# Kernel optimization log

Hardware: AMD Instinct MI355X
Metric: run time of the kernel (lower is better)

The kernel has to match this reference:

```python
import jax, jax.numpy as jnp
import numpy as np

NUM_MIXTURES = 10
DIM_INPUT = 512
DIM_FEATURES = 512
SEQ_LEN = 512
BATCH = 16
NUM_CHAR = 1024
DIM_CONTEXT = 256


def setup_inputs() -> dict:
    key = jax.random.key(0)
    ks = jax.random.split(key, 6)
    inputs = jax.random.normal(ks[0], (SEQ_LEN, BATCH, DIM_INPUT), dtype=jnp.float32)
    context_vectors = jax.random.normal(ks[1], (NUM_CHAR, BATCH, DIM_CONTEXT), dtype=jnp.float32)
    init_means = jnp.zeros((BATCH, NUM_MIXTURES), dtype=jnp.float32)
    # StackedLinearLayers params: 2 layers, leaky_relu between, out dim = 3*K
    s1 = 1.0 / np.sqrt(DIM_INPUT)
    s2 = 1.0 / np.sqrt(DIM_FEATURES)
    W1 = jax.random.uniform(ks[2], (DIM_INPUT, DIM_FEATURES), jnp.float32, -s1, s1)
    b1 = jax.random.uniform(ks[3], (DIM_FEATURES,), jnp.float32, -s1, s1)
    W2 = jax.random.uniform(ks[4], (DIM_FEATURES, 3 * NUM_MIXTURES), jnp.float32, -s2, s2)
    b2 = jax.random.uniform(ks[5], (3 * NUM_MIXTURES,), jnp.float32, -s2, s2)
    return dict(inputs=inputs, context_vectors=context_vectors, init_means=init_means,
                W1=W1, b1=b1, W2=W2, b2=b2, extra_chars=0)


def reference(inputs, context_vectors, init_means, W1, b1, W2, b2, extra_chars):
    K = NUM_MIXTURES
    seq_len, batch, _ = inputs.shape
    num_char = context_vectors.shape[0]
    total_char = num_char + extra_chars

    # StackedLinearLayers: leaky_relu MLP, last layer linear -> (S, B, 3K)
    h = jax.nn.leaky_relu(inputs @ W1 + b1, negative_slope=0.01)
    outs = h @ W2 + b2
    outs = jax.nn.softplus(outs)  # pos_fun = softplus

    delta_means, vars_, weights = jnp.split(outs, 3, axis=2)  # each (S, B, K)
    delta_means = delta_means / 25.0
    vars_ = jnp.clip(vars_, 0.01, 100.0)
    means = jnp.cumsum(delta_means, axis=0) + init_means[None, :, :]  # (S, B, K)

    cidxs = jnp.arange(total_char, dtype=jnp.float32)  # (T,)
    # dists: (S, B, K, T)
    dists = -((means[..., None] - cidxs) ** 2) * vars_[..., None]
    # attn_weights = exp(logsumexp over mixtures)
    attn_weights = jnp.exp(
        jax.scipy.special.logsumexp(jnp.log(weights)[..., None] + dists, axis=2)
    )  # (S, B, T)

    # attended contexts: (S, B, D)
    attn_contexts = jnp.einsum('sbc,cbd->sbd', attn_weights[:, :, :num_char], context_vectors)
    return attn_contexts, attn_weights, means, vars_, weights
```

## Files before the change

kernel.cpp:

```cpp
#include <hip/hip_runtime.h>
#include <math.h>

#define S_LEN 512
#define BATCH 16
#define DIN   512
#define DF    512
#define NMIX  10
#define NCHAR 1024
#define DCTX  256
#define M_ROWS (S_LEN*BATCH)

#define OFF_CTXOUT 0
#define OFF_ATTN   (S_LEN*BATCH*DCTX)
#define OFF_MEANS  (OFF_ATTN + S_LEN*BATCH*NCHAR)
#define OFF_VARS   (OFF_MEANS + S_LEN*BATCH*NMIX)
#define OFF_WTS    (OFF_VARS  + S_LEN*BATCH*NMIX)

#define WS_XH    0
#define WS_W1H   (8u<<20)
#define WS_W2T   (9u<<20)
#define WS_HH    (10u<<20)
#define WS_CTXH  (18u<<20)
#define WS_ATTNH (26u<<20)

#define NX4     1048576
#define NW14    65536
#define NCTX4   1048576
#define CVT4    (NX4 + NW14 + NCTX4)
#define CVT_BLOCKS (CVT4/256)
#define W2T_BLOCKS 64

typedef float    f32x16 __attribute__((ext_vector_type(16)));
typedef _Float16 f16x8  __attribute__((ext_vector_type(8)));

__device__ __forceinline__ unsigned short f2h(float x) {
    union { _Float16 h; unsigned short u; } cv;
    cv.h = (_Float16)x;
    return cv.u;
}
__device__ __forceinline__ ushort4 cvt4(float4 v) {
    ushort4 o; o.x = f2h(v.x); o.y = f2h(v.y); o.z = f2h(v.z); o.w = f2h(v.w);
    return o;
}

__global__ __launch_bounds__(256) void convert_kernel(
    const float* __restrict__ X, const float* __restrict__ W1,
    const float* __restrict__ ctx, const float* __restrict__ W2,
    unsigned short* __restrict__ Xh, unsigned short* __restrict__ W1h,
    unsigned short* __restrict__ ctxh, float* __restrict__ W2T)
{
    const int bid = blockIdx.x;
    if (bid < CVT_BLOCKS) {
        const int i4 = bid*256 + threadIdx.x;
        if (i4 < NX4) {
            ((ushort4*)Xh)[i4] = cvt4(((const float4*)X)[i4]);
        } else if (i4 < NX4 + NW14) {
            ((ushort4*)W1h)[i4 - NX4] = cvt4(((const float4*)W1)[i4 - NX4]);
        } else {
            const int j = i4 - NX4 - NW14;
            ((ushort4*)ctxh)[j] = cvt4(((const float4*)ctx)[j]);
        }
    } else {
        const int idx = (bid - CVT_BLOCKS)*256 + threadIdx.x;
        if (idx < 512*32) {
            const int j = idx >> 9, k = idx & 511;
            W2T[idx] = (j < 30) ? W2[k*30 + j] : 0.f;
        }
    }
}

__global__ __launch_bounds__(256) void gemm1_kernel(
    const unsigned short* __restrict__ Xh, const unsigned short* __restrict__ W1h,
    const float* __restrict__ b1, unsigned short* __restrict__ Hh)
{
    __shared__ __align__(16) unsigned short As[64*72];
    __shared__ __align__(16) unsigned short Bs[64*72];
    const int row0 = (blockIdx.x >> 3) * 64;
    const int n0   = (blockIdx.x & 7)  * 64;
    const int tid  = threadIdx.x;
    const int lane = tid & 63, w = tid >> 6;
    const int wr = (w >> 1) * 32, wc = (w & 1) * 32;
    const int m  = lane & 31,  g  = lane >> 5;
    const int sa = tid >> 2,   ka = (tid & 3) * 16;
    const int kb = tid & 63,   wb = tid >> 6;

    f32x16 acc = {};

    for (int kt = 0; kt < DIN; kt += 64) {
        uint4 av0 = *(const uint4*)(Xh  + (size_t)(row0+sa)*DIN + kt + ka);
        uint4 av1 = *(const uint4*)(Xh  + (size_t)(row0+sa)*DIN + kt + ka + 8);
        uint4 bv0 = *(const uint4*)(W1h + (size_t)(kt+kb)*DF + n0 + wb*16);
        uint4 bv1 = *(const uint4*)(W1h + (size_t)(kt+kb)*DF + n0 + wb*16 + 8);
        __syncthreads();
        *(uint4*)(As + sa*72 + ka)     = av0;
        *(uint4*)(As + sa*72 + ka + 8) = av1;
        {
            union { uint4 u; unsigned short s[8]; } p0, p1;
            p0.u = bv0; p1.u = bv1;
            #pragma unroll
            for (int i = 0; i < 8; i++) Bs[(wb*16 + i)*72 + kb]     = p0.s[i];
            #pragma unroll
            for (int i = 0; i < 8; i++) Bs[(wb*16 + 8 + i)*72 + kb] = p1.s[i];
        }
        __syncthreads();
        #pragma unroll
        for (int ks = 0; ks < 64; ks += 16) {
            f16x8 af = *(const f16x8*)(As + (wr+m)*72 + ks + g*8);
            f16x8 bf = *(const f16x8*)(Bs + (wc+m)*72 + ks + g*8);
            acc = __builtin_amdgcn_mfma_f32_32x32x16_f16(af, bf, acc, 0, 0, 0);
        }
    }
    const int ncol = n0 + wc + m;
    const float bb = b1[ncol];
    #pragma unroll
    for (int r = 0; r < 16; r++) {
        const int rowloc = (r & 3) + 8*(r >> 2) + 4*g;
        const int row = row0 + wr + rowloc;
        float v = acc[r] + bb;
        v = v > 0.f ? v : 0.01f * v;
        Hh[(size_t)row*DF + ncol] = f2h(v);
    }
}

__global__ __launch_bounds__(256) void gemm2_kernel(
    const unsigned short* __restrict__ Hh, const float* __restrict__ W2T,
    const float* __restrict__ b2,
    float* __restrict__ dmeans, float* __restrict__ dvars, float* __restrict__ dwts)
{
    __shared__ __align__(16) unsigned short Hs[32*520];
    const int tid = threadIdx.x;
    const int r0  = blockIdx.x * 32;
    {
        const uint4* src = (const uint4*)(Hh + (size_t)r0*DF);
        #pragma unroll
        for (int i = 0; i < 8; i++) {
            int u   = tid + i*256;
            int row = u >> 6;
            int col = (u & 63) * 8;
            *(uint4*)(Hs + row*520 + col) = src[u];
        }
    }
    __syncthreads();

    const int r  = tid & 31;
    const int j0 = tid >> 5;
    const unsigned short* hrow = Hs + r*520;
    float acc[4] = {0.f, 0.f, 0.f, 0.f};

    for (int k0 = 0; k0 < DF; k0 += 8) {
        union { uint4 u; _Float16 h[8]; } hv;
        hv.u = *(const uint4*)(hrow + k0);
        float wv[4][8];
        #pragma unroll
        for (int q = 0; q < 4; q++) {
            *(float4*)(wv[q])     = *(const float4*)(W2T + (size_t)(j0 + q*8)*DF + k0);
            *(float4*)(wv[q] + 4) = *(const float4*)(W2T + (size_t)(j0 + q*8)*DF + k0 + 4);
        }
        #pragma unroll
        for (int i = 0; i < 8; i++) {
            float hf = (float)hv.h[i];
            acc[0] = fmaf(hf, wv[0][i], acc[0]);
            acc[1] = fmaf(hf, wv[1][i], acc[1]);
            acc[2] = fmaf(hf, wv[2][i], acc[2]);
            acc[3] = fmaf(hf, wv[3][i], acc[3]);
        }
    }
    const int row = r0 + r;
    #pragma unroll
    for (int q = 0; q < 4; q++) {
        const int j = j0 + q*8;
        if (j >= 30) continue;
        float dot = acc[q] + b2[j];
        float sp  = fmaxf(dot, 0.f) + log1pf(__expf(-fabsf(dot)));
        if (j < 10)       dmeans[row*NMIX + j]      = sp / 25.0f;
        else if (j < 20)  dvars [row*NMIX + (j-10)] = fminf(fmaxf(sp, 0.01f), 100.f);
        else              dwts  [row*NMIX + (j-20)] = sp;
    }
}

__global__ __launch_bounds__(512) void scan_kernel(
    const float* __restrict__ init_means, float* __restrict__ means)
{
    const int p    = blockIdx.x;
    const int s    = threadIdx.x;
    const int lane = s & 63;
    const int wid  = s >> 6;

    float x = means[s*(BATCH*NMIX) + p];
    #pragma unroll
    for (int d = 1; d < 64; d <<= 1) {
        float tv = __shfl_up(x, d, 64);
        if (lane >= d) x += tv;
    }
    __shared__ float wsum[8];
    if (lane == 63) wsum[wid] = x;
    __syncthreads();
    float off = init_means[p];
    for (int i = 0; i < wid; i++) off += wsum[i];
    x += off;
    means[s*(BATCH*NMIX) + p] = x;
}

__global__ __launch_bounds__(256) void attn_kernel(
    const float* __restrict__ means, const float* __restrict__ vars,
    const float* __restrict__ wts,   float* __restrict__ attn,
    unsigned short* __restrict__ attnh)
{
    const int row = blockIdx.x;
    const int tid = threadIdx.x;
    float m[NMIX], v[NMIX], w[NMIX];
    #pragma unroll
    for (int k = 0; k < NMIX; k++) {
        m[k] = means[row*NMIX + k];
        v[k] = vars [row*NMIX + k];
        w[k] = wts  [row*NMIX + k];
    }
    const int t0 = tid * 4;
    float o[4];
    #pragma unroll
    for (int i = 0; i < 4; i++) {
        const float t = (float)(t0 + i);
        float sum = 0.f;
        #pragma unroll
        for (int k = 0; k < NMIX; k++) {
            float d = t - m[k];
            sum += w[k] * __expf(-d*d*v[k]);
        }
        o[i] = sum;
    }
    *(float4*)(attn + (size_t)row*NCHAR + t0) = make_float4(o[0],o[1],o[2],o[3]);
    ushort4 h; h.x = f2h(o[0]); h.y = f2h(o[1]); h.z = f2h(o[2]); h.w = f2h(o[3]);
    *(ushort4*)(attnh + (size_t)row*NCHAR + t0) = h;
}

__global__ __launch_bounds__(256) void ctx_mfma_kernel(
    const unsigned short* __restrict__ attnh, const unsigned short* __restrict__ ctxh,
    float* __restrict__ out)
{
    __shared__ __align__(16) unsigned short As[64*72];
    __shared__ __align__(16) unsigned short Bs[64*72];
    const int bid  = blockIdx.x;
    const int b    = bid >> 5;
    const int rem  = bid & 31;
    const int s0   = (rem >> 2) * 64;
    const int d0   = (rem & 3)  * 64;
    const int tid  = threadIdx.x;
    const int lane = tid & 63, w = tid >> 6;
    const int wr = (w >> 1) * 32, wc = (w & 1) * 32;
    const int m  = lane & 31,  g  = lane >> 5;
    const int sl = tid >> 2,   tq = (tid & 3) * 16;
    const int tb = tid & 63,   db = (tid >> 6) * 16;

    f32x16 acc = {};
    const unsigned short* abase = attnh + (size_t)(s0+sl)*(BATCH*NCHAR) + b*NCHAR + tq;
    const unsigned short* bbase = ctxh  + (size_t)b*DCTX + d0 + db;

    for (int kt = 0; kt < NCHAR; kt += 64) {
        uint4 a0 = *(const uint4*)(abase + kt);
        uint4 a1 = *(const uint4*)(abase + kt + 8);
        uint4 bv0 = *(const uint4*)(bbase + (size_t)(kt+tb)*(BATCH*DCTX));
        uint4 bv1 = *(const uint4*)(bbase + (size_t)(kt+tb)*(BATCH*DCTX) + 8);
        __syncthreads();
        *(uint4*)(As + sl*72 + tq)     = a0;
        *(uint4*)(As + sl*72 + tq + 8) = a1;
        {
            union { uint4 u; unsigned short s[8]; } p0, p1;
            p0.u = bv0; p1.u = bv1;
            #pragma unroll
            for (int i = 0; i < 8; i++) Bs[(db + i)*72 + tb]     = p0.s[i];
            #pragma unroll
            for (int i = 0; i < 8; i++) Bs[(db + 8 + i)*72 + tb] = p1.s[i];
        }
        __syncthreads();
        #pragma unroll
        for (int ks = 0; ks < 64; ks += 16) {
            f16x8 af = *(const f16x8*)(As + (wr+m)*72 + ks + g*8);
            f16x8 bf = *(const f16x8*)(Bs + (wc+m)*72 + ks + g*8);
            acc = __builtin_amdgcn_mfma_f32_32x32x16_f16(af, bf, acc, 0, 0, 0);
        }
    }
    #pragma unroll
    for (int r = 0; r < 16; r++) {
        int rowloc = (r & 3) + 8*(r >> 2) + 4*g;
        int s = s0 + wr + rowloc;
        out[(size_t)s*(BATCH*DCTX) + b*DCTX + d0 + wc + m] = acc[r];
    }
}

extern "C" void kernel_launch(void* const* d_in, const int* in_sizes, int n_in,
                              void* d_out, int out_size, void* d_ws, size_t ws_size,
                              hipStream_t stream)
{
    const float* X     = (const float*)d_in[0];
    const float* ctx   = (const float*)d_in[1];
    const float* initm = (const float*)d_in[2];
    const float* W1    = (const float*)d_in[3];
    const float* b1    = (const float*)d_in[4];
    const float* W2    = (const float*)d_in[5];
    const float* b2    = (const float*)d_in[6];

    float* out      = (float*)d_out;
    float* out_ctx  = out + OFF_CTXOUT;
    float* out_attn = out + OFF_ATTN;
    float* out_mean = out + OFF_MEANS;
    float* out_var  = out + OFF_VARS;
    float* out_wts  = out + OFF_WTS;

    char* ws = (char*)d_ws;
    unsigned short* Xh    = (unsigned short*)(ws + WS_XH);
    unsigned short* W1h   = (unsigned short*)(ws + WS_W1H);
    float*          W2T   = (float*)         (ws + WS_W2T);
    unsigned short* Hh    = (unsigned short*)(ws + WS_HH);
    unsigned short* ctxh  = (unsigned short*)(ws + WS_CTXH);
    unsigned short* attnh = (unsigned short*)(ws + WS_ATTNH);

    convert_kernel<<<CVT_BLOCKS + W2T_BLOCKS, 256, 0, stream>>>(
        X, W1, ctx, W2, Xh, W1h, ctxh, W2T);
    gemm1_kernel<<<(M_ROWS/64)*(DF/64), 256, 0, stream>>>(Xh, W1h, b1, Hh);
    gemm2_kernel<<<M_ROWS/32, 256, 0, stream>>>(Hh, W2T, b2, out_mean, out_var, out_wts);
    scan_kernel<<<BATCH*NMIX, 512, 0, stream>>>(initm, out_mean);
    attn_kernel<<<M_ROWS, 256, 0, stream>>>(out_mean, out_var, out_wts, out_attn, attnh);
    ctx_mfma_kernel<<<16*8*4, 256, 0, stream>>>(attnh, ctxh, out_ctx);
}
```

Measured before the change: 172.1 us.

## Fuse cumulative-sum scan into attention kernel, recomputing the scan per block

Removes the separate scan kernel and the old per-row attention kernel, replacing them with one kernel per (batch, 32-char tile). Each block loads the deltas, vars and weights for all 512 sequence steps of its batch, performs the prefix scan itself, stages the parameters in shared memory and computes attention for its char tile. This drops one launch and the global round trip for the means. In exchange the scan is recomputed redundantly 32 times per batch, and the attn stores become 4-byte and 2-byte scalars with only 32-element contiguity.

```diff
diff --git a/kernel.cpp b/kernel.cpp
--- a/kernel.cpp
+++ b/kernel.cpp
@@ -22,6 +22,7 @@
 #define WS_HH    (10u<<20)
 #define WS_CTXH  (18u<<20)
 #define WS_ATTNH (26u<<20)
+#define WS_DELTA (44u<<20)
 
 #define NX4     1048576
 #define NW14    65536
@@ -125,7 +126,7 @@
 __global__ __launch_bounds__(256) void gemm2_kernel(
     const unsigned short* __restrict__ Hh, const float* __restrict__ W2T,
     const float* __restrict__ b2,
-    float* __restrict__ dmeans, float* __restrict__ dvars, float* __restrict__ dwts)
+    float* __restrict__ deltas, float* __restrict__ dvars, float* __restrict__ dwts)
 {
     __shared__ __align__(16) unsigned short Hs[32*520];
     const int tid = threadIdx.x;
@@ -172,65 +173,100 @@
         if (j >= 30) continue;
         float dot = acc[q] + b2[j];
         float sp  = fmaxf(dot, 0.f) + log1pf(__expf(-fabsf(dot)));
-        if (j < 10)       dmeans[row*NMIX + j]      = sp / 25.0f;
+        if (j < 10)       deltas[row*NMIX + j]      = sp / 25.0f;
         else if (j < 20)  dvars [row*NMIX + (j-10)] = fminf(fmaxf(sp, 0.01f), 100.f);
         else              dwts  [row*NMIX + (j-20)] = sp;
     }
 }
 
-__global__ __launch_bounds__(512) void scan_kernel(
-    const float* __restrict__ init_means, float* __restrict__ means)
-{
-    const int p    = blockIdx.x;
-    const int s    = threadIdx.x;
-    const int lane = s & 63;
-    const int wid  = s >> 6;
-
-    float x = means[s*(BATCH*NMIX) + p];
-    #pragma unroll
-    for (int d = 1; d < 64; d <<= 1) {
-        float tv = __shfl_up(x, d, 64);
-        if (lane >= d) x += tv;
-    }
-    __shared__ float wsum[8];
-    if (lane == 63) wsum[wid] = x;
+__global__ __launch_bounds__(512) void attn_fused_kernel(
+    const float* __restrict__ deltas, const float* __restrict__ initm,
+    const float* __restrict__ vars_g, const float* __restrict__ wts_g,
+    float* __restrict__ means_out, float* __restrict__ attn,
+    unsigned short* __restrict__ attnh)
+{
+    __shared__ __align__(16) float mvw[256*36];
+    __shared__ float wsum[8][NMIX];
+    const int bid  = blockIdx.x;
+    const int b    = bid >> 5;
+    const int tc   = bid & 31;
+    const int tid  = threadIdx.x;
+    const int lane = tid & 63, wid = tid >> 6;
+    const int row  = tid*BATCH + b;
+
+    float d[NMIX], vv[NMIX], ww[NMIX];
+    #pragma unroll
+    for (int k = 0; k < NMIX; k++) d[k]  = deltas[row*NMIX + k];
+    #pragma unroll
+    for (int k = 0; k < NMIX; k++) vv[k] = vars_g[row*NMIX + k];
+    #pragma unroll
+    for (int k = 0; k < NMIX; k++) ww[k] = wts_g[row*NMIX + k];
+
+    #pragma unroll
+    for (int k = 0; k < NMIX; k++) {
+        #pragma unroll
+        for (int dd = 1; dd < 64; dd <<= 1) {
+            float t = __shfl_up(d[k], dd, 64);
+            if (lane >= dd) d[k] += t;
+        }
+    }
+    if (lane == 63) {
+        #pragma unroll
+        for (int k = 0; k < NMIX; k++) wsum[wid][k] = d[k];
+    }
     __syncthreads();
-    float off = init_means[p];
-    for (int i = 0; i < wid; i++) off += wsum[i];
-    x += off;
-    means[s*(BATCH*NMIX) + p] = x;
-}
-
-__global__ __launch_bounds__(256) void attn_kernel(
-    const float* __restrict__ means, const float* __restrict__ vars,
-    const float* __restrict__ wts,   float* __restrict__ attn,
-    unsigned short* __restrict__ attnh)
-{
-    const int row = blockIdx.x;
-    const int tid = threadIdx.x;
-    float m[NMIX], v[NMIX], w[NMIX];
     #pragma unroll
     for (int k = 0; k < NMIX; k++) {
-        m[k] = means[row*NMIX + k];
-        v[k] = vars [row*NMIX + k];
-        w[k] = wts  [row*NMIX + k];
-    }
-    const int t0 = tid * 4;
-    float o[4];
-    #pragma unroll
-    for (int i = 0; i < 4; i++) {
-        const float t = (float)(t0 + i);
-        float sum = 0.f;
-        #pragma unroll
-        for (int k = 0; k < NMIX; k++) {
-            float d = t - m[k];
-            sum += w[k] * __expf(-d*d*v[k]);
-        }
-        o[i] = sum;
-    }
-    *(float4*)(attn + (size_t)row*NCHAR + t0) = make_float4(o[0],o[1],o[2],o[3]);
-    ushort4 h; h.x = f2h(o[0]); h.y = f2h(o[1]); h.z = f2h(o[2]); h.w = f2h(o[3]);
-    *(ushort4*)(attnh + (size_t)row*NCHAR + t0) = h;
+        float base = initm[b*NMIX + k];
+        for (int w2 = 0; w2 < wid; w2++) base += wsum[w2][k];
+        d[k] += base;
+    }
+    if (tc == 0) {
+        #pragma unroll
+        for (int k = 0; k < NMIX; k++) means_out[row*NMIX + k] = d[k];
+    }
+
+    const int   t_idx = tc*32 + (tid & 31);
+    const float tf    = (float)t_idx;
+    const int   s_off = tid >> 5;
+
+    for (int half = 0; half < 2; half++) {
+        __syncthreads();
+        if ((tid >> 8) == half) {
+            const int sl = tid & 255;
+            #pragma unroll
+            for (int k = 0; k < NMIX; k++) mvw[sl*36 + k]      = d[k];
+            #pragma unroll
+            for (int k = 0; k < NMIX; k++) mvw[sl*36 + 12 + k] = vv[k];
+            #pragma unroll
+            for (int k = 0; k < NMIX; k++) mvw[sl*36 + 24 + k] = ww[k];
+        }
+        __syncthreads();
+        for (int si = 0; si < 256; si += 16) {
+            const int sl = si + s_off;
+            const int s  = half*256 + sl;
+            const float* p = &mvw[sl*36];
+            float m[NMIX], v[NMIX], w[NMIX];
+            *(float4*)(m)     = *(const float4*)(p);
+            *(float4*)(m + 4) = *(const float4*)(p + 4);
+            *(float2*)(m + 8) = *(const float2*)(p + 8);
+            *(float4*)(v)     = *(const float4*)(p + 12);
+            *(float4*)(v + 4) = *(const float4*)(p + 16);
+            *(float2*)(v + 8) = *(const float2*)(p + 20);
+            *(float4*)(w)     = *(const float4*)(p + 24);
+            *(float4*)(w + 4) = *(const float4*)(p + 28);
+            *(float2*)(w + 8) = *(const float2*)(p + 32);
+            float sum = 0.f;
+            #pragma unroll
+            for (int k = 0; k < NMIX; k++) {
+                float dd = tf - m[k];
+                sum += w[k] * __expf(-dd*dd*v[k]);
+            }
+            const size_t o = (size_t)(s*BATCH + b)*NCHAR + t_idx;
+            attn[o]  = sum;
+            attnh[o] = f2h(sum);
+        }
+    }
 }
 
 __global__ __launch_bounds__(256) void ctx_mfma_kernel(
@@ -256,8 +292,8 @@
     const unsigned short* bbase = ctxh  + (size_t)b*DCTX + d0 + db;
 
     for (int kt = 0; kt < NCHAR; kt += 64) {
-        uint4 a0 = *(const uint4*)(abase + kt);
-        uint4 a1 = *(const uint4*)(abase + kt + 8);
+        uint4 a0  = *(const uint4*)(abase + kt);
+        uint4 a1  = *(const uint4*)(abase + kt + 8);
         uint4 bv0 = *(const uint4*)(bbase + (size_t)(kt+tb)*(BATCH*DCTX));
         uint4 bv1 = *(const uint4*)(bbase + (size_t)(kt+tb)*(BATCH*DCTX) + 8);
         __syncthreads();
@@ -313,12 +349,13 @@
     unsigned short* Hh    = (unsigned short*)(ws + WS_HH);
     unsigned short* ctxh  = (unsigned short*)(ws + WS_CTXH);
     unsigned short* attnh = (unsigned short*)(ws + WS_ATTNH);
+    float*          delt  = (float*)         (ws + WS_DELTA);
 
     convert_kernel<<<CVT_BLOCKS + W2T_BLOCKS, 256, 0, stream>>>(
         X, W1, ctx, W2, Xh, W1h, ctxh, W2T);
     gemm1_kernel<<<(M_ROWS/64)*(DF/64), 256, 0, stream>>>(Xh, W1h, b1, Hh);
-    gemm2_kernel<<<M_ROWS/32, 256, 0, stream>>>(Hh, W2T, b2, out_mean, out_var, out_wts);
-    scan_kernel<<<BATCH*NMIX, 512, 0, stream>>>(initm, out_mean);
-    attn_kernel<<<M_ROWS, 256, 0, stream>>>(out_mean, out_var, out_wts, out_attn, attnh);
+    gemm2_kernel<<<M_ROWS/32, 256, 0, stream>>>(Hh, W2T, b2, delt, out_var, out_wts);
+    attn_fused_kernel<<<BATCH*32, 512, 0, stream>>>(
+        delt, initm, out_var, out_wts, out_mean, out_attn, attnh);
     ctx_mfma_kernel<<<16*8*4, 256, 0, stream>>>(attnh, ctxh, out_ctx);
 }
```

New measurement: 179.1 us. +4.0%, slower.

## Bound attention support per batch and truncate attn and context GEMM range

Applied to the files above, without the earlier changes.

The scan kernel now computes, for each batch, an upper bound on character positions with non-negligible attention: the maximum of mean + 4.8/sqrt(var) across sequence and mixtures. It publishes this with an atomicMax into a workspace buffer that the convert kernel zeroes. The attention kernel skips the exp evaluation beyond this bound and writes zeros there. The context GEMM limits its K loop to the bound rounded up to 64. This removes most of the Gaussian evaluations and most of the reduction work in the context GEMM. The cost is a small truncation error, around exp(-23) relative, and a reliance on means only increasing, since no lower bound is applied.

```diff
diff --git a/kernel.cpp b/kernel.cpp
--- a/kernel.cpp
+++ b/kernel.cpp
@@ -22,6 +22,7 @@
 #define WS_HH    (10u<<20)
 #define WS_CTXH  (18u<<20)
 #define WS_ATTNH (26u<<20)
+#define WS_BOUND (44u<<20)
 
 #define NX4     1048576
 #define NW14    65536
@@ -47,7 +48,8 @@
     const float* __restrict__ X, const float* __restrict__ W1,
     const float* __restrict__ ctx, const float* __restrict__ W2,
     unsigned short* __restrict__ Xh, unsigned short* __restrict__ W1h,
-    unsigned short* __restrict__ ctxh, float* __restrict__ W2T)
+    unsigned short* __restrict__ ctxh, float* __restrict__ W2T,
+    unsigned int* __restrict__ bound)
 {
     const int bid = blockIdx.x;
     if (bid < CVT_BLOCKS) {
@@ -60,12 +62,14 @@
             const int j = i4 - NX4 - NW14;
             ((ushort4*)ctxh)[j] = cvt4(((const float4*)ctx)[j]);
         }
-    } else {
+    } else if (bid < CVT_BLOCKS + W2T_BLOCKS) {
         const int idx = (bid - CVT_BLOCKS)*256 + threadIdx.x;
         if (idx < 512*32) {
             const int j = idx >> 9, k = idx & 511;
             W2T[idx] = (j < 30) ? W2[k*30 + j] : 0.f;
         }
+    } else {
+        if (threadIdx.x < BATCH) bound[threadIdx.x] = 0u;
     }
 }
 
@@ -179,7 +183,8 @@
 }
 
 __global__ __launch_bounds__(512) void scan_kernel(
-    const float* __restrict__ init_means, float* __restrict__ means)
+    const float* __restrict__ init_means, float* __restrict__ means,
+    const float* __restrict__ vars_g, unsigned int* __restrict__ bound)
 {
     const int p    = blockIdx.x;
     const int s    = threadIdx.x;
@@ -193,49 +198,72 @@
         if (lane >= d) x += tv;
     }
     __shared__ float wsum[8];
+    __shared__ float wmax[8];
     if (lane == 63) wsum[wid] = x;
     __syncthreads();
     float off = init_means[p];
     for (int i = 0; i < wid; i++) off += wsum[i];
     x += off;
     means[s*(BATCH*NMIX) + p] = x;
+
+    float v = vars_g[s*(BATCH*NMIX) + p];
+    float reach = x + 4.8f * rsqrtf(v);
+    #pragma unroll
+    for (int d = 32; d >= 1; d >>= 1)
+        reach = fmaxf(reach, __shfl_xor(reach, d, 64));
+    if (lane == 0) wmax[wid] = reach;
+    __syncthreads();
+    if (s == 0) {
+        float mx = wmax[0];
+        #pragma unroll
+        for (int i = 1; i < 8; i++) mx = fmaxf(mx, wmax[i]);
+        atomicMax((int*)&bound[p / NMIX], __float_as_int(mx));
+    }
 }
 
 __global__ __launch_bounds__(256) void attn_kernel(
     const float* __restrict__ means, const float* __restrict__ vars,
-    const float* __restrict__ wts,   float* __restrict__ attn,
-    unsigned short* __restrict__ attnh)
+    const float* __restrict__ wts,   const unsigned int* __restrict__ bound,
+    float* __restrict__ attn, unsigned short* __restrict__ attnh)
 {
     const int row = blockIdx.x;
+    const int b   = row & (BATCH-1);
     const int tid = threadIdx.x;
-    float m[NMIX], v[NMIX], w[NMIX];
-    #pragma unroll
-    for (int k = 0; k < NMIX; k++) {
-        m[k] = means[row*NMIX + k];
-        v[k] = vars [row*NMIX + k];
-        w[k] = wts  [row*NMIX + k];
-    }
-    const int t0 = tid * 4;
-    float o[4];
-    #pragma unroll
-    for (int i = 0; i < 4; i++) {
-        const float t = (float)(t0 + i);
-        float sum = 0.f;
+    const int bd  = (int)__int_as_float((int)bound[b]);
+    const int kmax = min(NCHAR, (bd + 64) & ~63);
+    const int t0  = tid * 4;
+
+    float o[4] = {0.f, 0.f, 0.f, 0.f};
+    if (t0 <= bd) {
+        float m[NMIX], v[NMIX], w[NMIX];
         #pragma unroll
         for (int k = 0; k < NMIX; k++) {
-            float d = t - m[k];
-            sum += w[k] * __expf(-d*d*v[k]);
-        }
-        o[i] = sum;
+            m[k] = means[row*NMIX + k];
+            v[k] = vars [row*NMIX + k];
+            w[k] = wts  [row*NMIX + k];
+        }
+        #pragma unroll
+        for (int i = 0; i < 4; i++) {
+            const float t = (float)(t0 + i);
+            float sum = 0.f;
+            #pragma unroll
+            for (int k = 0; k < NMIX; k++) {
+                float d = t - m[k];
+                sum += w[k] * __expf(-d*d*v[k]);
+            }
+            o[i] = sum;
+        }
     }
     *(float4*)(attn + (size_t)row*NCHAR + t0) = make_float4(o[0],o[1],o[2],o[3]);
-    ushort4 h; h.x = f2h(o[0]); h.y = f2h(o[1]); h.z = f2h(o[2]); h.w = f2h(o[3]);
-    *(ushort4*)(attnh + (size_t)row*NCHAR + t0) = h;
+    if (t0 < kmax) {
+        ushort4 h; h.x = f2h(o[0]); h.y = f2h(o[1]); h.z = f2h(o[2]); h.w = f2h(o[3]);
+        *(ushort4*)(attnh + (size_t)row*NCHAR + t0) = h;
+    }
 }
 
 __global__ __launch_bounds__(256) void ctx_mfma_kernel(
     const unsigned short* __restrict__ attnh, const unsigned short* __restrict__ ctxh,
-    float* __restrict__ out)
+    const unsigned int* __restrict__ bound, float* __restrict__ out)
 {
     __shared__ __align__(16) unsigned short As[64*72];
     __shared__ __align__(16) unsigned short Bs[64*72];
@@ -251,13 +279,16 @@
     const int sl = tid >> 2,   tq = (tid & 3) * 16;
     const int tb = tid & 63,   db = (tid >> 6) * 16;
 
+    const int bd   = (int)__int_as_float((int)bound[b]);
+    const int kmax = min(NCHAR, (bd + 64) & ~63);
+
     f32x16 acc = {};
     const unsigned short* abase = attnh + (size_t)(s0+sl)*(BATCH*NCHAR) + b*NCHAR + tq;
     const unsigned short* bbase = ctxh  + (size_t)b*DCTX + d0 + db;
 
-    for (int kt = 0; kt < NCHAR; kt += 64) {
-        uint4 a0 = *(const uint4*)(abase + kt);
-        uint4 a1 = *(const uint4*)(abase + kt + 8);
+    for (int kt = 0; kt < kmax; kt += 64) {
+        uint4 a0  = *(const uint4*)(abase + kt);
+        uint4 a1  = *(const uint4*)(abase + kt + 8);
         uint4 bv0 = *(const uint4*)(bbase + (size_t)(kt+tb)*(BATCH*DCTX));
         uint4 bv1 = *(const uint4*)(bbase + (size_t)(kt+tb)*(BATCH*DCTX) + 8);
         __syncthreads();
@@ -313,12 +344,14 @@
     unsigned short* Hh    = (unsigned short*)(ws + WS_HH);
     unsigned short* ctxh  = (unsigned short*)(ws + WS_CTXH);
     unsigned short* attnh = (unsigned short*)(ws + WS_ATTNH);
-
-    convert_kernel<<<CVT_BLOCKS + W2T_BLOCKS, 256, 0, stream>>>(
-        X, W1, ctx, W2, Xh, W1h, ctxh, W2T);
+    unsigned int*   bnd   = (unsigned int*)  (ws + WS_BOUND);
+
+    convert_kernel<<<CVT_BLOCKS + W2T_BLOCKS + 1, 256, 0, stream>>>(
+        X, W1, ctx, W2, Xh, W1h, ctxh, W2T, bnd);
     gemm1_kernel<<<(M_ROWS/64)*(DF/64), 256, 0, stream>>>(Xh, W1h, b1, Hh);
     gemm2_kernel<<<M_ROWS/32, 256, 0, stream>>>(Hh, W2T, b2, out_mean, out_var, out_wts);
-    scan_kernel<<<BATCH*NMIX, 512, 0, stream>>>(initm, out_mean);
-    attn_kernel<<<M_ROWS, 256, 0, stream>>>(out_mean, out_var, out_wts, out_attn, attnh);
-    ctx_mfma_kernel<<<16*8*4, 256, 0, stream>>>(attnh, ctxh, out_ctx);
-}
+    scan_kernel<<<BATCH*NMIX, 512, 0, stream>>>(initm, out_mean, out_var, bnd);
+    attn_kernel<<<M_ROWS, 256, 0, stream>>>(out_mean, out_var, out_wts, bnd,
+                                            out_attn, attnh);
+    ctx_mfma_kernel<<<16*8*4, 256, 0, stream>>>(attnh, ctxh, bnd, out_ctx);
+}
```

After: 152.2 us. 11.6% less time.
